# Optimization experiments

Measured on AMD Instinct MI355X. Metric: run time of the kernel, lower is better.

The kernel has to match this reference:

```python
import jax, jax.numpy as jnp
import numpy as np

N, D, NUM_IDS = 4096, 2048, 256
MARGIN = 0.3


def _pairwise_euclidean(x):
    # torch.cdist(x, x, p=2): safe sqrt of squared distances (zero-grad at 0)
    sq = jnp.sum(x * x, axis=1)                      # [N]
    d2 = sq[:, None] + sq[None, :] - 2.0 * (x @ x.T)  # [N, N]
    d2 = jnp.maximum(d2, 0.0)
    d = jnp.sqrt(jnp.where(d2 > 0.0, d2, 1.0))
    return jnp.where(d2 > 0.0, d, 0.0)


def setup_inputs() -> dict:
    key = jax.random.key(0)
    k1, k2 = jax.random.split(key)
    features = jax.random.normal(k1, (N, D), dtype=jnp.float32)
    labels = jax.random.randint(k2, (N,), 0, NUM_IDS, dtype=jnp.int64)
    return {"features": features, "labels": labels}


def reference(features, labels):
    dist = _pairwise_euclidean(features)                     # [N, N]
    mask_pos = labels[None, :] == labels[:, None]            # [N, N] bool
    # batch-hard mining: hardest positive (max), hardest negative (min)
    dist_ap = jnp.max(jnp.where(mask_pos, dist, 0.0), axis=1)       # [N]
    dist_an = jnp.min(jnp.where(mask_pos, jnp.inf, dist), axis=1)   # [N]
    valid = (dist_ap > 0.0) & jnp.isfinite(dist_an)
    # MarginRankingLoss(dist_an, dist_ap, y=1) = mean(relu(dist_ap - dist_an + margin))
    per_anchor = jnp.maximum(dist_ap - dist_an + MARGIN, 0.0)
    n_valid = jnp.sum(valid)
    loss = jnp.sum(jnp.where(valid, per_anchor, 0.0)) / jnp.maximum(n_valid, 1).astype(per_anchor.dtype)
    return jnp.where(n_valid > 0, loss, 0.0)
```

## Files before the change

### kernel.cpp

```cpp
#include <hip/hip_runtime.h>

#define NN 4096
#define DD 2048
#define MARGIN_F 0.3f
#define NTILES 1056
#define BK 256
#define NIT (DD / BK)
#define QS (127.0f / 6.0f)
#define C2 (2.0f * (6.0f / 127.0f) * (6.0f / 127.0f))

typedef __attribute__((ext_vector_type(4))) int i32x4;

__device__ __forceinline__ unsigned q8(float v) {
    int i = __float2int_rn(v * QS);
    i = min(127, max(-127, i));
    return (unsigned)(i & 255);
}

__global__ __launch_bounds__(256) void prep_kernel(const float* __restrict__ x,
                                                   unsigned char* __restrict__ xq,
                                                   float* __restrict__ sq,
                                                   unsigned int* __restrict__ ap,
                                                   unsigned int* __restrict__ an,
                                                   int* __restrict__ counter) {
    const int wave = threadIdx.x >> 6, lane = threadIdx.x & 63;
    const int row = blockIdx.x * 4 + wave;
    const float* xr = x + (size_t)row * DD;
    unsigned int* orow = (unsigned int*)(xq + (size_t)row * DD);
    float s = 0.0f;
#pragma unroll
    for (int j = 0; j < 8; ++j) {
        float4 v = ((const float4*)xr)[j * 64 + lane];
        s += v.x * v.x + v.y * v.y + v.z * v.z + v.w * v.w;
        orow[j * 64 + lane] = q8(v.x) | (q8(v.y) << 8) | (q8(v.z) << 16) | (q8(v.w) << 24);
    }
    for (int off = 32; off > 0; off >>= 1) s += __shfl_down(s, off, 64);
    if (lane == 0) {
        sq[row] = s;
        ap[row] = 0u;
        an[row] = 0x7F800000u;
    }
    if (threadIdx.x == 0 && blockIdx.x == 0) counter[0] = 0;
}

__global__ __launch_bounds__(256) void gemm_reduce_kernel(
    const unsigned char* __restrict__ xq,
    const float* __restrict__ sq,
    const int* __restrict__ labels,
    unsigned int* __restrict__ ap,
    unsigned int* __restrict__ an,
    int* __restrict__ counter,
    float* __restrict__ out) {
    __shared__ __align__(16) unsigned char As[64 * BK];
    __shared__ __align__(16) unsigned char Bs[128 * BK];

    int rem = blockIdx.x;
    int mi64 = 0;
    while (rem >= 32 - (mi64 >> 1)) { rem -= 32 - (mi64 >> 1); ++mi64; }
    const int nj = (mi64 >> 1) + rem;
    const int row0 = mi64 * 64;
    const int col0 = nj * 128;
    const int phase = blockIdx.x & (NIT - 1);

    const int t = threadIdx.x;
    const int lane = t & 63;
    const int wave = t >> 6;
    const int c = lane & 15;
    const int q = lane >> 4;
    const int wc = wave * 32;

    i32x4 acc[4][2];
#pragma unroll
    for (int mi = 0; mi < 4; ++mi)
#pragma unroll
        for (int ni = 0; ni < 2; ++ni)
            acc[mi][ni] = (i32x4){0, 0, 0, 0};

    const int rowb = t >> 4;
    const int colsw = (t & 15) ^ (rowb & 15);
    const unsigned char* gA[4];
    const unsigned char* gB[8];
#pragma unroll
    for (int s = 0; s < 4; ++s)
        gA[s] = xq + (size_t)(row0 + rowb + 16 * s) * DD + colsw * 16;
#pragma unroll
    for (int s = 0; s < 8; ++s)
        gB[s] = xq + (size_t)(col0 + rowb + 16 * s) * DD + colsw * 16;

    for (int it = 0; it < NIT; ++it) {
        const int k0 = ((it + phase) & (NIT - 1)) * BK;
#pragma unroll
        for (int s = 0; s < 4; ++s)
            __builtin_amdgcn_global_load_lds(
                (const __attribute__((address_space(1))) void*)(gA[s] + k0),
                (__attribute__((address_space(3))) void*)&As[(t + 256 * s) * 16],
                16, 0, 0);
#pragma unroll
        for (int s = 0; s < 8; ++s)
            __builtin_amdgcn_global_load_lds(
                (const __attribute__((address_space(1))) void*)(gB[s] + k0),
                (__attribute__((address_space(3))) void*)&Bs[(t + 256 * s) * 16],
                16, 0, 0);
        __syncthreads();

        const i32x4* Av = (const i32x4*)As;
        const i32x4* Bv = (const i32x4*)Bs;
#pragma unroll
        for (int ks = 0; ks < 4; ++ks) {
            const int kc = q + 4 * ks;
            i32x4 af[4], bfr[2];
#pragma unroll
            for (int mi = 0; mi < 4; ++mi) {
                const int r = mi * 16 + c;
                af[mi] = Av[r * 16 + (kc ^ (r & 15))];
            }
#pragma unroll
            for (int ni = 0; ni < 2; ++ni) {
                const int r = wc + ni * 16 + c;
                bfr[ni] = Bv[r * 16 + (kc ^ (r & 15))];
            }
#pragma unroll
            for (int mi = 0; mi < 4; ++mi)
#pragma unroll
                for (int ni = 0; ni < 2; ++ni)
                    acc[mi][ni] = __builtin_amdgcn_mfma_i32_16x16x64_i8(
                        af[mi], bfr[ni], acc[mi][ni], 0, 0, 0);
        }
        __syncthreads();
    }

    float sq_col[2];
    int lab_col[2];
#pragma unroll
    for (int ni = 0; ni < 2; ++ni) {
        const int gj = col0 + wc + ni * 16 + c;
        sq_col[ni] = sq[gj];
        lab_col[ni] = labels[gj];
    }
    int lab_row[4][4];
    float dist[4][2][4];
#pragma unroll
    for (int mi = 0; mi < 4; ++mi) {
#pragma unroll
        for (int r = 0; r < 4; ++r) {
            const int gi = row0 + mi * 16 + q * 4 + r;
            const float sqi = sq[gi];
            lab_row[mi][r] = labels[gi];
#pragma unroll
            for (int ni = 0; ni < 2; ++ni) {
                float d2 = sqi + sq_col[ni] - C2 * (float)acc[mi][ni][r];
                dist[mi][ni][r] = sqrtf(fmaxf(d2, 0.0f));
            }
        }
    }

#pragma unroll
    for (int mi = 0; mi < 4; ++mi) {
#pragma unroll
        for (int r = 0; r < 4; ++r) {
            const int gi = row0 + mi * 16 + q * 4 + r;
            const int li = lab_row[mi][r];
            float apm = 0.0f;
            float anm = __builtin_inff();
#pragma unroll
            for (int ni = 0; ni < 2; ++ni) {
                const int gj = col0 + wc + ni * 16 + c;
                const float d = dist[mi][ni][r];
                if (li == lab_col[ni]) {
                    if (gi != gj) apm = fmaxf(apm, d);
                } else {
                    anm = fminf(anm, d);
                }
            }
#pragma unroll
            for (int off = 1; off < 16; off <<= 1) {
                apm = fmaxf(apm, __shfl_xor(apm, off, 16));
                anm = fminf(anm, __shfl_xor(anm, off, 16));
            }
            if (c == 0) {
                atomicMax(&ap[gi], __float_as_uint(apm));
                atomicMin(&an[gi], __float_as_uint(anm));
            }
        }
    }

#pragma unroll
    for (int ni = 0; ni < 2; ++ni) {
        const int gj = col0 + wc + ni * 16 + c;
        const int lj = lab_col[ni];
        float apm = 0.0f;
        float anm = __builtin_inff();
#pragma unroll
        for (int mi = 0; mi < 4; ++mi) {
#pragma unroll
            for (int r = 0; r < 4; ++r) {
                const int gi = row0 + mi * 16 + q * 4 + r;
                const float d = dist[mi][ni][r];
                if (lj == lab_row[mi][r]) {
                    if (gi != gj) apm = fmaxf(apm, d);
                } else {
                    anm = fminf(anm, d);
                }
            }
        }
        apm = fmaxf(apm, __shfl_xor(apm, 16, 64));
        anm = fminf(anm, __shfl_xor(anm, 16, 64));
        apm = fmaxf(apm, __shfl_xor(apm, 32, 64));
        anm = fminf(anm, __shfl_xor(anm, 32, 64));
        if (q == 0) {
            atomicMax(&ap[gj], __float_as_uint(apm));
            atomicMin(&an[gj], __float_as_uint(anm));
        }
    }

    __syncthreads();
    int* flag = (int*)As;
    if (t == 0) {
        int old = __hip_atomic_fetch_add(counter, 1, __ATOMIC_ACQ_REL,
                                         __HIP_MEMORY_SCOPE_AGENT);
        flag[0] = (old == NTILES - 1) ? 1 : 0;
    }
    __syncthreads();
    if (flag[0]) {
        float sum = 0.0f;
        int cnt = 0;
        for (int i = t; i < NN; i += 256) {
            const float a = __uint_as_float(__hip_atomic_load(
                &ap[i], __ATOMIC_RELAXED, __HIP_MEMORY_SCOPE_AGENT));
            const float b = __uint_as_float(__hip_atomic_load(
                &an[i], __ATOMIC_RELAXED, __HIP_MEMORY_SCOPE_AGENT));
            if ((a > 0.0f) && (b < __builtin_inff())) {
                sum += fmaxf(a - b + MARGIN_F, 0.0f);
                cnt += 1;
            }
        }
        for (int off = 32; off > 0; off >>= 1) {
            sum += __shfl_down(sum, off, 64);
            cnt += __shfl_down(cnt, off, 64);
        }
        float* ssum = (float*)Bs;
        int* scnt = (int*)Bs + 8;
        if (lane == 0) { ssum[wave] = sum; scnt[wave] = cnt; }
        __syncthreads();
        if (t == 0) {
            float s = 0.0f; int n = 0;
#pragma unroll
            for (int w = 0; w < 4; ++w) { s += ssum[w]; n += scnt[w]; }
            out[0] = (n > 0) ? s / (float)n : 0.0f;
        }
    }
}

extern "C" void kernel_launch(void* const* d_in, const int* in_sizes, int n_in,
                              void* d_out, int out_size, void* d_ws, size_t ws_size,
                              hipStream_t stream) {
    const float* x = (const float*)d_in[0];
    const int* labels = (const int*)d_in[1];
    float* out = (float*)d_out;

    char* ws = (char*)d_ws;
    unsigned char* xq = (unsigned char*)ws;
    float* sq = (float*)(ws + (size_t)NN * DD);
    unsigned int* ap = (unsigned int*)(ws + (size_t)NN * DD + (size_t)NN * 4);
    unsigned int* an = (unsigned int*)(ws + (size_t)NN * DD + (size_t)NN * 8);
    int* counter = (int*)(ws + (size_t)NN * DD + (size_t)NN * 12);

    prep_kernel<<<NN / 4, 256, 0, stream>>>(x, xq, sq, ap, an, counter);
    gemm_reduce_kernel<<<NTILES, 256, 0, stream>>>(xq, sq, labels, ap, an, counter, out);
}
```

Before: 142.3 us.

## Double-buffer LDS tiles with half-size K chunks and remap workgroups across XCDs

Halves the K chunk to 128 bytes and adds a second LDS buffer pair, so the global-to-LDS load of the next chunk is issued before computing the current one. This lets loads overlap the MFMA work instead of waiting behind a barrier each iteration. It also permutes the block index so consecutive tiles map to the same XCD (orig&7 striding), which is meant to improve L2 reuse of shared row and column panels. Total LDS stays the same, but there are twice as many barriers and a smaller swizzle width (8).

Measured after the change: 150.5 us. +5.8%, slower.

```diff
diff --git a/kernel.cpp b/kernel.cpp
--- a/kernel.cpp
+++ b/kernel.cpp
@@ -4,7 +4,7 @@
 #define DD 2048
 #define MARGIN_F 0.3f
 #define NTILES 1056
-#define BK 256
+#define BK 128
 #define NIT (DD / BK)
 #define QS (127.0f / 6.0f)
 #define C2 (2.0f * (6.0f / 127.0f) * (6.0f / 127.0f))
@@ -51,16 +51,21 @@
     unsigned int* __restrict__ an,
     int* __restrict__ counter,
     float* __restrict__ out) {
-    __shared__ __align__(16) unsigned char As[64 * BK];
-    __shared__ __align__(16) unsigned char Bs[128 * BK];
-
-    int rem = blockIdx.x;
+    __shared__ __align__(16) unsigned char As0[64 * BK];
+    __shared__ __align__(16) unsigned char Bs0[128 * BK];
+    __shared__ __align__(16) unsigned char As1[64 * BK];
+    __shared__ __align__(16) unsigned char Bs1[128 * BK];
+
+    const int orig = blockIdx.x;
+    const int wgid = (orig & 7) * (NTILES / 8) + (orig >> 3);
+
+    int rem = wgid;
     int mi64 = 0;
     while (rem >= 32 - (mi64 >> 1)) { rem -= 32 - (mi64 >> 1); ++mi64; }
     const int nj = (mi64 >> 1) + rem;
     const int row0 = mi64 * 64;
     const int col0 = nj * 128;
-    const int phase = blockIdx.x & (NIT - 1);
+    const int phase = wgid & (NIT - 1);
 
     const int t = threadIdx.x;
     const int lane = t & 63;
@@ -76,48 +81,49 @@
         for (int ni = 0; ni < 2; ++ni)
             acc[mi][ni] = (i32x4){0, 0, 0, 0};
 
-    const int rowb = t >> 4;
-    const int colsw = (t & 15) ^ (rowb & 15);
-    const unsigned char* gA[4];
-    const unsigned char* gB[8];
+    const int rowb = t >> 3;
+    const int colsw = (t & 7) ^ (rowb & 7);
+    const unsigned char* gA[2];
+    const unsigned char* gB[4];
+#pragma unroll
+    for (int s = 0; s < 2; ++s)
+        gA[s] = xq + (size_t)(row0 + rowb + 32 * s) * DD + colsw * 16;
 #pragma unroll
     for (int s = 0; s < 4; ++s)
-        gA[s] = xq + (size_t)(row0 + rowb + 16 * s) * DD + colsw * 16;
-#pragma unroll
-    for (int s = 0; s < 8; ++s)
-        gB[s] = xq + (size_t)(col0 + rowb + 16 * s) * DD + colsw * 16;
-
-    for (int it = 0; it < NIT; ++it) {
+        gB[s] = xq + (size_t)(col0 + rowb + 32 * s) * DD + colsw * 16;
+
+    auto stage = [&](unsigned char* A, unsigned char* B, int it) {
         const int k0 = ((it + phase) & (NIT - 1)) * BK;
+#pragma unroll
+        for (int s = 0; s < 2; ++s)
+            __builtin_amdgcn_global_load_lds(
+                (const __attribute__((address_space(1))) void*)(gA[s] + k0),
+                (__attribute__((address_space(3))) void*)&A[(t + 256 * s) * 16],
+                16, 0, 0);
 #pragma unroll
         for (int s = 0; s < 4; ++s)
             __builtin_amdgcn_global_load_lds(
-                (const __attribute__((address_space(1))) void*)(gA[s] + k0),
-                (__attribute__((address_space(3))) void*)&As[(t + 256 * s) * 16],
+                (const __attribute__((address_space(1))) void*)(gB[s] + k0),
+                (__attribute__((address_space(3))) void*)&B[(t + 256 * s) * 16],
                 16, 0, 0);
-#pragma unroll
-        for (int s = 0; s < 8; ++s)
-            __builtin_amdgcn_global_load_lds(
-                (const __attribute__((address_space(1))) void*)(gB[s] + k0),
-                (__attribute__((address_space(3))) void*)&Bs[(t + 256 * s) * 16],
-                16, 0, 0);
-        __syncthreads();
-
-        const i32x4* Av = (const i32x4*)As;
-        const i32x4* Bv = (const i32x4*)Bs;
-#pragma unroll
-        for (int ks = 0; ks < 4; ++ks) {
+    };
+
+    auto compute = [&](const unsigned char* A, const unsigned char* B) {
+        const i32x4* Av = (const i32x4*)A;
+        const i32x4* Bv = (const i32x4*)B;
+#pragma unroll
+        for (int ks = 0; ks < 2; ++ks) {
             const int kc = q + 4 * ks;
             i32x4 af[4], bfr[2];
 #pragma unroll
             for (int mi = 0; mi < 4; ++mi) {
                 const int r = mi * 16 + c;
-                af[mi] = Av[r * 16 + (kc ^ (r & 15))];
+                af[mi] = Av[r * 8 + (kc ^ (r & 7))];
             }
 #pragma unroll
             for (int ni = 0; ni < 2; ++ni) {
                 const int r = wc + ni * 16 + c;
-                bfr[ni] = Bv[r * 16 + (kc ^ (r & 15))];
+                bfr[ni] = Bv[r * 8 + (kc ^ (r & 7))];
             }
 #pragma unroll
             for (int mi = 0; mi < 4; ++mi)
@@ -126,6 +132,16 @@
                     acc[mi][ni] = __builtin_amdgcn_mfma_i32_16x16x64_i8(
                         af[mi], bfr[ni], acc[mi][ni], 0, 0, 0);
         }
+    };
+
+    stage(As0, Bs0, 0);
+    __syncthreads();
+    for (int it = 0; it < NIT; it += 2) {
+        stage(As1, Bs1, it + 1);
+        compute(As0, Bs0);
+        __syncthreads();
+        if (it + 2 < NIT) stage(As0, Bs0, it + 2);
+        compute(As1, Bs1);
         __syncthreads();
     }
 
@@ -214,7 +230,7 @@
     }
 
     __syncthreads();
-    int* flag = (int*)As;
+    int* flag = (int*)As0;
     if (t == 0) {
         int old = __hip_atomic_fetch_add(counter, 1, __ATOMIC_ACQ_REL,
                                          __HIP_MEMORY_SCOPE_AGENT);
@@ -238,8 +254,8 @@
             sum += __shfl_down(sum, off, 64);
             cnt += __shfl_down(cnt, off, 64);
         }
-        float* ssum = (float*)Bs;
-        int* scnt = (int*)Bs + 8;
+        float* ssum = (float*)Bs0;
+        int* scnt = (int*)Bs0 + 8;
         if (lane == 0) { ssum[wave] = sum; scnt[wave] = cnt; }
         __syncthreads();
         if (t == 0) {
```
